# Optimization experiments

Measured on AMD Instinct MI355X. Metric: run time of the kernel, lower is better.

## Reference

```python
import jax, jax.numpy as jnp
import numpy as np

N1, N2, D = 8192, 8192, 8

def setup_inputs() -> dict:
    key = jax.random.key(0)
    k1, k2 = jax.random.split(key)
    input1 = jax.random.uniform(k1, (N1, D), dtype=jnp.float32)
    input2 = jax.random.uniform(k2, (N2, D), dtype=jnp.float32)
    gamma = jnp.array(1.0, dtype=jnp.float32)
    return {"input1": input1, "input2": input2, "gamma": gamma}

def reference(input1, input2, gamma):
    # array[i, j] = exp((sum_d (input1[i,d] - input2[j,d]))**2) * gamma
    # sum_d (x_i - c_j) = rowsum(x)_i - rowsum(c)_j, so reduce first then broadcast.
    s1 = jnp.sum(input1, axis=1)  # (N1,)
    s2 = jnp.sum(input2, axis=1)  # (N2,)
    diff = s1[:, None] - s2[None, :]  # (N1, N2)
    return jnp.exp(diff * diff) * gamma
```

## Files before the change

### kernel.cpp

```cpp
#include <hip/hip_runtime.h>


#define N1 8192
#define N2 8192
#define D  8
#define ROWS 32

typedef float f32x4 __attribute__((ext_vector_type(4)));

__device__ __forceinline__ float rowsum8(const float* __restrict__ p) {
    const f32x4* q = reinterpret_cast<const f32x4*>(p);
    f32x4 a = q[0];
    f32x4 b = q[1];
    return ((a.x + a.y) + (a.z + a.w)) + ((b.x + b.y) + (b.z + b.w));
}

__global__ void __launch_bounds__(256)
rbf_fused_kernel(const float* __restrict__ in1,
                 const float* __restrict__ in2,
                 const float* __restrict__ gamma_p,
                 f32x4* __restrict__ out) {
    const int cb = blockIdx.x;
    const int rb = blockIdx.y;
    const int t  = threadIdx.x;

    __shared__ float s1s[ROWS];

    const int col0 = cb * 1024 + t * 4;
    float s20 = rowsum8(in2 + (size_t)(col0 + 0) * D);
    float s21 = rowsum8(in2 + (size_t)(col0 + 1) * D);
    float s22 = rowsum8(in2 + (size_t)(col0 + 2) * D);
    float s23 = rowsum8(in2 + (size_t)(col0 + 3) * D);

    if (t < ROWS) {
        s1s[t] = rowsum8(in1 + (size_t)(rb * ROWS + t) * D);
    }
    const float g = gamma_p[0];
    __syncthreads();

    f32x4* __restrict__ orow = out + (size_t)(rb * ROWS) * (N2 / 4) + cb * 256 + t;

    #pragma unroll 4
    for (int r = 0; r < ROWS; ++r) {
        const float s1 = s1s[r];
        float d0 = s1 - s20;
        float d1 = s1 - s21;
        float d2 = s1 - s22;
        float d3 = s1 - s23;
        f32x4 v;
        v.x = __expf(d0 * d0) * g;
        v.y = __expf(d1 * d1) * g;
        v.z = __expf(d2 * d2) * g;
        v.w = __expf(d3 * d3) * g;
        __builtin_nontemporal_store(v, orow);
        orow += N2 / 4;
    }
}

extern "C" void kernel_launch(void* const* d_in, const int* in_sizes, int n_in,
                              void* d_out, int out_size, void* d_ws, size_t ws_size,
                              hipStream_t stream) {
    const float* in1     = (const float*)d_in[0];
    const float* in2     = (const float*)d_in[1];
    const float* gamma_p = (const float*)d_in[2];
    f32x4* out = (f32x4*)d_out;

    dim3 block(256);
    dim3 grid(N2 / 1024, N1 / ROWS);
    rbf_fused_kernel<<<grid, block, 0, stream>>>(in1, in2, gamma_p, out);
}
```

Baseline: 49.05 us.

## Precompute row sums in a separate kernel and widen main kernel to full rows

Splits the work into a small kernel that computes all row sums of both inputs into workspace, and a main kernel where each block covers 32 full output rows with 32 column sums held in registers per thread. This removes the redundant recomputation of input2 row sums across row blocks and the shared-memory sync. The cost is an extra kernel launch, a dependency through global memory, and a grid of only 256 blocks, which may limit latency hiding on a GPU with many compute units.

```diff
diff --git a/kernel.cpp b/kernel.cpp
--- a/kernel.cpp
+++ b/kernel.cpp
@@ -5,6 +5,7 @@
 #define N2 8192
 #define D  8
 #define ROWS 32
+#define NBLK (N1 / ROWS)
 
 typedef float f32x4 __attribute__((ext_vector_type(4)));
 
@@ -15,45 +16,53 @@
     return ((a.x + a.y) + (a.z + a.w)) + ((b.x + b.y) + (b.z + b.w));
 }
 
+__global__ void rbf_rowsum_kernel(const float* __restrict__ in1,
+                                  const float* __restrict__ in2,
+                                  float* __restrict__ s) {
+    int idx = blockIdx.x * blockDim.x + threadIdx.x;
+    if (idx < N1) {
+        s[idx] = rowsum8(in1 + (size_t)idx * D);
+    } else if (idx < N1 + N2) {
+        int j = idx - N1;
+        s[N1 + j] = rowsum8(in2 + (size_t)j * D);
+    }
+}
+
 __global__ void __launch_bounds__(256)
-rbf_fused_kernel(const float* __restrict__ in1,
-                 const float* __restrict__ in2,
-                 const float* __restrict__ gamma_p,
-                 f32x4* __restrict__ out) {
-    const int cb = blockIdx.x;
-    const int rb = blockIdx.y;
+rbf_main_kernel(const float* __restrict__ s,
+                const float* __restrict__ gamma_p,
+                f32x4* __restrict__ out) {
+    const int rb = blockIdx.x;
     const int t  = threadIdx.x;
 
-    __shared__ float s1s[ROWS];
+    const f32x4* s2v4 = reinterpret_cast<const f32x4*>(s + N1);
+    f32x4 s2r[8];
+    #pragma unroll
+    for (int c = 0; c < 8; ++c) s2r[c] = s2v4[c * 256 + t];
 
-    const int col0 = cb * 1024 + t * 4;
-    float s20 = rowsum8(in2 + (size_t)(col0 + 0) * D);
-    float s21 = rowsum8(in2 + (size_t)(col0 + 1) * D);
-    float s22 = rowsum8(in2 + (size_t)(col0 + 2) * D);
-    float s23 = rowsum8(in2 + (size_t)(col0 + 3) * D);
+    const float g = gamma_p[0];
+    const float* s1p = s + rb * ROWS;
 
-    if (t < ROWS) {
-        s1s[t] = rowsum8(in1 + (size_t)(rb * ROWS + t) * D);
-    }
-    const float g = gamma_p[0];
-    __syncthreads();
+    f32x4* __restrict__ obase = out + (size_t)rb * ROWS * (N2 / 4) + t;
 
-    f32x4* __restrict__ orow = out + (size_t)(rb * ROWS) * (N2 / 4) + cb * 256 + t;
-
-    #pragma unroll 4
+    #pragma unroll 2
     for (int r = 0; r < ROWS; ++r) {
-        const float s1 = s1s[r];
-        float d0 = s1 - s20;
-        float d1 = s1 - s21;
-        float d2 = s1 - s22;
-        float d3 = s1 - s23;
-        f32x4 v;
-        v.x = __expf(d0 * d0) * g;
-        v.y = __expf(d1 * d1) * g;
-        v.z = __expf(d2 * d2) * g;
-        v.w = __expf(d3 * d3) * g;
-        __builtin_nontemporal_store(v, orow);
-        orow += N2 / 4;
+        const float s1 = s1p[r];
+        f32x4* __restrict__ orow = obase + (size_t)r * (N2 / 4);
+        #pragma unroll
+        for (int c = 0; c < 8; ++c) {
+            f32x4 sv = s2r[c];
+            float d0 = s1 - sv.x;
+            float d1 = s1 - sv.y;
+            float d2 = s1 - sv.z;
+            float d3 = s1 - sv.w;
+            f32x4 v;
+            v.x = __expf(d0 * d0) * g;
+            v.y = __expf(d1 * d1) * g;
+            v.z = __expf(d2 * d2) * g;
+            v.w = __expf(d3 * d3) * g;
+            __builtin_nontemporal_store(v, orow + c * 256);
+        }
     }
 }
 
@@ -63,9 +72,15 @@
     const float* in1     = (const float*)d_in[0];
     const float* in2     = (const float*)d_in[1];
     const float* gamma_p = (const float*)d_in[2];
+    float* ws  = (float*)d_ws;
     f32x4* out = (f32x4*)d_out;
 
-    dim3 block(256);
-    dim3 grid(N2 / 1024, N1 / ROWS);
-    rbf_fused_kernel<<<grid, block, 0, stream>>>(in1, in2, gamma_p, out);
+    {
+        const int threads = 256;
+        const int blocks  = (N1 + N2 + threads - 1) / threads;
+        rbf_rowsum_kernel<<<blocks, threads, 0, stream>>>(in1, in2, ws);
+    }
+    {
+        rbf_main_kernel<<<NBLK, 256, 0, stream>>>(ws, gamma_p, out);
+    }
 }
```

After: 59.86 us. 1.22x slower.
